# Optimization experiments

Hardware: AMD Instinct MI355X
Metric: run time of the kernel (lower is better)

Reference implementation:

```python
import jax, jax.numpy as jnp
import numpy as np

BETA = 1.0  # config.beta
B, G, K, E2 = 1024, 512, 128, 128


def setup_inputs() -> dict:
    key = jax.random.key(0)
    k1, k2, k3, k4, k5 = jax.random.split(key, 5)
    s = 0.05
    return {
        "images": jax.random.normal(k1, (B, G), dtype=jnp.float32),
        "wimg": jax.random.normal(k2, (G, K), dtype=jnp.float32) * s,    # project.weight.T
        "wrec": jax.random.normal(k3, (K, E2), dtype=jnp.float32) * s,   # rec.weight.T
        "wrec2": jax.random.normal(k4, (K + 1, E2), dtype=jnp.float32) * s,  # rec2.weight.T
        "wimg2": jax.random.normal(k5, (G, K, K + 1), dtype=jnp.float32) * s,  # img2.weight.T.reshape(K+1,K,G).T
    }


def _soft_assign(x, codes):
    # x: [B, D], codes: [D, C] -> softmax over C of -beta * mean_D (x - codes)^2
    xh = -jnp.mean((x[:, :, None] - codes[None]) ** 2, axis=1) * BETA  # [B, C]
    return jax.nn.softmax(xh, axis=-1)


def reference(images, wimg, wrec, wrec2, wimg2):
    # ---- encode ----
    xp = _soft_assign(images, wimg)            # [B, K]
    lat = xp @ wrec                            # [B, E2]
    xp = _soft_assign(lat, wrec.T)             # [B, K] (codes are wrec.T: [E2, K])
    idx = jnp.argmax(xp, axis=-1)              # [B] hard component
    xwimg = jnp.transpose(wimg2[:, idx, :], (1, 0, 2))   # [B, G, K+1]
    base = wimg[:, idx].T[:, :, None]                     # [B, G, 1]
    xd = images[:, :, None] - base - xwimg                # [B, G, K+1]
    xh2 = -jnp.mean(xd ** 2, axis=1) * BETA               # [B, K+1]
    xp2 = jax.nn.softmax(xh2, axis=-1)
    lat2 = xp2 @ wrec2                                    # [B, E2]
    # ---- decode (ret='rec', n_step>=1) ----
    xp_d = _soft_assign(lat, wrec.T)           # [B, K]
    xp2_d = _soft_assign(lat2, wrec2.T)        # [B, K+1]
    wimgg = wimg[:, :, None] + wimg2           # [G, K, K+1]
    # tensordot(xp_d[:, :, None]*xp2_d[:, None, :], wimgg.permute(1,2,0), 2)
    xrec = jnp.einsum('bk,bj,gkj->bg', xp_d, xp2_d, wimgg)  # [B, G]
    # ---- loss ----
    loss = jnp.mean((xrec - images) ** 2, axis=-1)  # [B]
    return loss
```

## Files before the change

kernel.cpp:

```cpp
#include <hip/hip_runtime.h>

#define B_    1024
#define G_    512
#define K_    128
#define J_    129
#define JP_   132
#define E2_   128
#define KK_   16512
#define KK2_  16896
#define KKE2_ 17024
#define KKP_  17408
#define SPLITS 16
#define KCHUNK 1088
#define BK_   32
#define KSTEPS 34
#define GS_   8

using short8 = __attribute__((ext_vector_type(8))) short;
using f32x4  = __attribute__((ext_vector_type(4))) float;

__device__ __forceinline__ float bf2f(unsigned short h){
  return __uint_as_float(((unsigned int)h) << 16);
}
__device__ __forceinline__ unsigned short f2bf(float f){
  unsigned int u = __float_as_uint(f);
  u += 0x7fffu + ((u >> 16) & 1u);
  return (unsigned short)(u >> 16);
}

#define GLOAD16(gptr, ldst) __builtin_amdgcn_global_load_lds( \
    (const __attribute__((address_space(1))) unsigned int*)(gptr), \
    (__attribute__((address_space(3))) unsigned int*)(ldst), 16, 0, 0)

__device__ __forceinline__ void blockSum2(float v0, float v1, float* red, int t,
                                          float& r0, float& r1){
  #pragma unroll
  for (int off = 32; off > 0; off >>= 1){
    v0 += __shfl_down(v0, off);
    v1 += __shfl_down(v1, off);
  }
  __syncthreads();
  if ((t & 63) == 0){ red[t >> 6] = v0; red[8 + (t >> 6)] = v1; }
  __syncthreads();
  r0 = ((red[0] + red[1]) + (red[2] + red[3])) + ((red[4] + red[5]) + (red[6] + red[7]));
  r1 = ((red[8] + red[9]) + (red[10] + red[11])) + ((red[12] + red[13]) + (red[14] + red[15]));
  __syncthreads();
}

__device__ __forceinline__ void blockSoftmaxMS2(float x0, float x1, bool act,
    float* redm, float* reds, int t,
    float& m0o, float& s0o, float& m1o, float& s1o){
  float m0 = x0, s0 = act ? 1.f : 0.f;
  float m1 = x1, s1 = act ? 1.f : 0.f;
  #pragma unroll
  for (int off = 32; off > 0; off >>= 1){
    float om0 = __shfl_down(m0, off), os0 = __shfl_down(s0, off);
    float om1 = __shfl_down(m1, off), os1 = __shfl_down(s1, off);
    float nm0 = fmaxf(m0, om0);
    s0 = s0*__expf(m0 - nm0) + os0*__expf(om0 - nm0); m0 = nm0;
    float nm1 = fmaxf(m1, om1);
    s1 = s1*__expf(m1 - nm1) + os1*__expf(om1 - nm1); m1 = nm1;
  }
  __syncthreads();
  if ((t & 63) == 0){
    redm[t >> 6] = m0; reds[t >> 6] = s0;
    redm[8 + (t >> 6)] = m1; reds[8 + (t >> 6)] = s1;
  }
  __syncthreads();
  float gm0 = redm[0], gs0 = reds[0], gm1 = redm[8], gs1 = reds[8];
  #pragma unroll
  for (int w = 1; w < 8; w++){
    float om0 = redm[w], os0 = reds[w];
    float nm0 = fmaxf(gm0, om0);
    gs0 = gs0*__expf(gm0 - nm0) + os0*__expf(om0 - nm0); gm0 = nm0;
    float om1 = redm[8 + w], os1 = reds[8 + w];
    float nm1 = fmaxf(gm1, om1);
    gs1 = gs1*__expf(gm1 - nm1) + os1*__expf(om1 - nm1); gm1 = nm1;
  }
  m0o = gm0; s0o = gs0; m1o = gm1; s1o = gs1;
}

__device__ __forceinline__ void blockSoftmaxMSI2(float x0, float x1, int idx, bool act,
    float* redm, float* reds, int* redi, int t,
    float& m0o, float& s0o, int& i0o, float& m1o, float& s1o, int& i1o){
  float m0 = x0, s0 = act ? 1.f : 0.f; int i0 = idx;
  float m1 = x1, s1 = act ? 1.f : 0.f; int i1 = idx;
  #pragma unroll
  for (int off = 32; off > 0; off >>= 1){
    float om0 = __shfl_down(m0, off), os0 = __shfl_down(s0, off);
    int   oi0 = __shfl_down(i0, off);
    float om1 = __shfl_down(m1, off), os1 = __shfl_down(s1, off);
    int   oi1 = __shfl_down(i1, off);
    bool tk0 = (om0 > m0) || (om0 == m0 && oi0 < i0);
    float nm0 = fmaxf(m0, om0);
    s0 = s0*__expf(m0 - nm0) + os0*__expf(om0 - nm0);
    i0 = tk0 ? oi0 : i0; m0 = nm0;
    bool tk1 = (om1 > m1) || (om1 == m1 && oi1 < i1);
    float nm1 = fmaxf(m1, om1);
    s1 = s1*__expf(m1 - nm1) + os1*__expf(om1 - nm1);
    i1 = tk1 ? oi1 : i1; m1 = nm1;
  }
  __syncthreads();
  if ((t & 63) == 0){
    redm[t >> 6] = m0; reds[t >> 6] = s0; redi[t >> 6] = i0;
    redm[8 + (t >> 6)] = m1; reds[8 + (t >> 6)] = s1; redi[8 + (t >> 6)] = i1;
  }
  __syncthreads();
  float gm0 = redm[0], gs0 = reds[0]; int gi0 = redi[0];
  float gm1 = redm[8], gs1 = reds[8]; int gi1 = redi[8];
  #pragma unroll
  for (int w = 1; w < 8; w++){
    { float om = redm[w], os = reds[w]; int oi = redi[w];
      bool tk = (om > gm0) || (om == gm0 && oi < gi0);
      float nm = fmaxf(gm0, om);
      gs0 = gs0*__expf(gm0 - nm) + os*__expf(om - nm);
      gi0 = tk ? oi : gi0; gm0 = nm; }
    { float om = redm[8 + w], os = reds[8 + w]; int oi = redi[8 + w];
      bool tk = (om > gm1) || (om == gm1 && oi < gi1);
      float nm = fmaxf(gm1, om);
      gs1 = gs1*__expf(gm1 - nm) + os*__expf(om - nm);
      gi1 = tk ? oi : gi1; gm1 = nm; }
  }
  m0o = gm0; s0o = gs0; i0o = gi0; m1o = gm1; s1o = gs1; i1o = gi1;
}

__global__ __launch_bounds__(1024) void norms_kernel(
    const float* __restrict__ wimg, const float* __restrict__ wrec,
    const float* __restrict__ wrec2, float* __restrict__ c1norm,
    float* __restrict__ w3norm, float* __restrict__ w6norm,
    float* __restrict__ wrecT, float* __restrict__ wrec2T){
  int t = threadIdx.x;
  if (blockIdx.x == 0){
    __shared__ float red[8][128];
    int k = t & 127, sl = t >> 7;
    float s = 0.f;
    int g0 = sl * (G_/8);
    for (int g = g0; g < g0 + G_/8; g++){
      float v = wimg[g*K_ + k]; s += v*v;
    }
    red[sl][k] = s;
    __syncthreads();
    if (t < 128){
      float r = 0.f;
      #pragma unroll
      for (int i = 0; i < 8; i++) r += red[i][t];
      c1norm[t] = r;
    }
  } else if (blockIdx.x == 1){
    int wave = t >> 6, lane = t & 63;
    for (int k = wave; k < K_; k += 16){
      float v0 = wrec[k*E2_ + lane], v1 = wrec[k*E2_ + 64 + lane];
      float s = v0*v0 + v1*v1;
      #pragma unroll
      for (int off = 32; off > 0; off >>= 1) s += __shfl_down(s, off);
      if (lane == 0) w3norm[k] = s;
    }
  } else if (blockIdx.x == 2){
    int wave = t >> 6, lane = t & 63;
    for (int j = wave; j < J_; j += 16){
      float v0 = wrec2[j*E2_ + lane], v1 = wrec2[j*E2_ + 64 + lane];
      float s = v0*v0 + v1*v1;
      #pragma unroll
      for (int off = 32; off > 0; off >>= 1) s += __shfl_down(s, off);
      if (lane == 0) w6norm[j] = s;
    }
  } else if (blockIdx.x == 3){
    for (int n = t; n < K_*E2_; n += 1024){
      int k = n >> 7, e = n & 127;
      wrecT[e*K_ + k] = wrec[n];
    }
  } else {
    for (int n = t; n < J_*E2_; n += 1024){
      int j = n >> 7, e = n & 127;
      wrec2T[e*J_ + j] = wrec2[n];
    }
  }
}

__global__ __launch_bounds__(128) void tables_part_kernel(
    const float* __restrict__ wimg2, const float* __restrict__ wimg,
    float* __restrict__ sqp, float* __restrict__ crp,
    unsigned short* __restrict__ W2){
  int n  = blockIdx.x * 128 + threadIdx.x;
  int gs = blockIdx.y;
  int k = n / J_;
  int w2i = n + 3*k;
  float s0=0,s1=0,s2=0,s3=0, c0=0,c1=0,c2=0,c3=0;
  int gbase = gs * (G_/GS_);
  #pragma unroll 2
  for (int g = gbase; g < gbase + G_/GS_; g += 4){
    float w0 = wimg2[(size_t)(g  )*KK_ + n];
    float w1 = wimg2[(size_t)(g+1)*KK_ + n];
    float w2 = wimg2[(size_t)(g+2)*KK_ + n];
    float w3 = wimg2[(size_t)(g+3)*KK_ + n];
    W2[(size_t)(g  )*KKP_ + w2i] = f2bf(w0);
    W2[(size_t)(g+1)*KKP_ + w2i] = f2bf(w1);
    W2[(size_t)(g+2)*KKP_ + w2i] = f2bf(w2);
    W2[(size_t)(g+3)*KKP_ + w2i] = f2bf(w3);
    s0 += w0*w0; s1 += w1*w1; s2 += w2*w2; s3 += w3*w3;
    c0 += wimg[(g  )*K_ + k]*w0;
    c1 += wimg[(g+1)*K_ + k]*w1;
    c2 += wimg[(g+2)*K_ + k]*w2;
    c3 += wimg[(g+3)*K_ + k]*w3;
  }
  sqp[(size_t)gs*KK_ + n] = (s0+s1)+(s2+s3);
  crp[(size_t)gs*KK_ + n] = (c0+c1)+(c2+c3);
}
__global__ __launch_bounds__(128) void tables_reduce_kernel(
    const float* __restrict__ sqp, const float* __restrict__ crp,
    float* __restrict__ sq2, float* __restrict__ cross){
  int n = blockIdx.x * 128 + threadIdx.x;
  float s = 0.f, c = 0.f;
  #pragma unroll
  for (int gs = 0; gs < GS_; gs++){
    s += sqp[(size_t)gs*KK_ + n];
    c += crp[(size_t)gs*KK_ + n];
  }
  sq2[n] = s; cross[n] = c;
}

__global__ __launch_bounds__(128) void w2tail_kernel(
    const float* __restrict__ wimg, unsigned short* __restrict__ W2){
  int g = blockIdx.x, t = threadIdx.x;
  unsigned short* dst = W2 + (size_t)g * KKP_;
  dst[KK2_ + t]        = f2bf(wimg[g*K_ + t]);
  dst[KKE2_ + t]       = 0;
  dst[KKE2_ + 128 + t] = 0;
  dst[KKE2_ + 256 + t] = 0;
  dst[t*JP_ + 129] = 0;
  dst[t*JP_ + 130] = 0;
  dst[t*JP_ + 131] = 0;
}

__global__ __launch_bounds__(512, 4) void encdec_kernel(
    const float* __restrict__ img,  const float* __restrict__ wimg,
    const float* __restrict__ wrec, const float* __restrict__ wrec2,
    const float* __restrict__ wrecT, const float* __restrict__ wrec2T,
    const unsigned short* __restrict__ W2,
    const float* __restrict__ c1norm, const float* __restrict__ w3norm,
    const float* __restrict__ w6norm, const float* __restrict__ sq2,
    const float* __restrict__ cross, unsigned short* __restrict__ Rm){
  __shared__ __align__(16) float simg[2][G_];
  __shared__ float sp[2][K_];
  __shared__ float sqv[2][JP_];
  __shared__ float slat[2][E2_];
  __shared__ float sd1[2][K_];
  __shared__ __align__(16) float sh16a[16][128];
  __shared__ __align__(16) float sh16b[16][128];
  __shared__ float sh4a[4][K_], sh4b[4][K_];
  __shared__ float xtra[4];
  __shared__ float redm[16], reds[16];
  __shared__ int   redi[16];

  int t = threadIdx.x;
  int b0 = blockIdx.x * 2, b1 = b0 + 1;
  int tt = t & 127, q = t >> 7;
  int ll = t & 31, gq = t >> 5;
  int wvid = t >> 6, lane = t & 63;

  simg[0][t] = img[b0*G_ + t];
  simg[1][t] = img[b1*G_ + t];
  __syncthreads();
  float a0 = simg[0][t], a1 = simg[1][t];
  float in0, in1;
  blockSum2(a0*a0, a1*a1, redm, t, in0, in1);

  {
    float p00=0,p01=0,p02=0,p03=0, p10=0,p11=0,p12=0,p13=0;
    int g0 = gq * 32;
    #pragma unroll 4
    for (int g = g0; g < g0 + 32; g++){
      float4 wv = *(const float4*)(wimg + g*K_ + 4*ll);
      float sv0 = simg[0][g], sv1 = simg[1][g];
      p00 += sv0*wv.x; p01 += sv0*wv.y; p02 += sv0*wv.z; p03 += sv0*wv.w;
      p10 += sv1*wv.x; p11 += sv1*wv.y; p12 += sv1*wv.z; p13 += sv1*wv.w;
    }
    float4 st0 = {p00,p01,p02,p03};
    float4 st1 = {p10,p11,p12,p13};
    *(float4*)&sh16a[gq][4*ll] = st0;
    *(float4*)&sh16b[gq][4*ll] = st1;
  }
  __syncthreads();
  float xh10 = -3e38f, xh11 = -3e38f;
  if (t < 128){
    float d0 = 0.f, d1 = 0.f;
    #pragma unroll
    for (int i = 0; i < 16; i++){ d0 += sh16a[i][t]; d1 += sh16b[i][t]; }
    sd1[0][t] = d0; sd1[1][t] = d1;
    xh10 = -(in0 - 2.f*d0 + c1norm[t]) * (1.f/512.f);
    xh11 = -(in1 - 2.f*d1 + c1norm[t]) * (1.f/512.f);
  }
  float m10, s10, m11, s11;
  blockSoftmaxMS2(xh10, xh11, t < 128, redm, reds, t, m10, s10, m11, s11);
  if (t < 128){
    sp[0][t] = __expf(xh10 - m10) / s10;
    sp[1][t] = __expf(xh11 - m11) / s11;
  }
  __syncthreads();

  {
    float l00=0,l01=0, l10=0,l11=0;
    int k0 = q * 32;
    for (int k = k0; k < k0 + 32; k += 2){
      float w0 = wrec[(k  )*E2_ + tt];
      float w1 = wrec[(k+1)*E2_ + tt];
      l00 += sp[0][k]*w0; l01 += sp[0][k+1]*w1;
      l10 += sp[1][k]*w0; l11 += sp[1][k+1]*w1;
    }
    sh4a[q][tt] = l00 + l01;
    sh4b[q][tt] = l10 + l11;
  }
  __syncthreads();
  float lat0 = (sh4a[0][tt] + sh4a[1][tt]) + (sh4a[2][tt] + sh4a[3][tt]);
  float lat1 = (sh4b[0][tt] + sh4b[1][tt]) + (sh4b[2][tt] + sh4b[3][tt]);
  if (q == 0){ slat[0][tt] = lat0; slat[1][tt] = lat1; }
  float ln0, ln1;
  blockSum2((q == 0) ? lat0*lat0 : 0.f, (q == 0) ? lat1*lat1 : 0.f, redm, t, ln0, ln1);

  {
    float l00=0,l01=0, l10=0,l11=0;
    int e0 = q * 32;
    const float* rT = wrecT + tt;
    for (int e = e0; e < e0 + 32; e += 2){
      float w0 = rT[(e  )*K_];
      float w1 = rT[(e+1)*K_];
      l00 += slat[0][e]*w0; l01 += slat[0][e+1]*w1;
      l10 += slat[1][e]*w0; l11 += slat[1][e+1]*w1;
    }
    sh4a[q][tt] = l00 + l01;
    sh4b[q][tt] = l10 + l11;
  }
  __syncthreads();
  float xh30 = -3e38f, xh31 = -3e38f;
  if (t < 128){
    float d30 = (sh4a[0][t] + sh4a[1][t]) + (sh4a[2][t] + sh4a[3][t]);
    float d31 = (sh4b[0][t] + sh4b[1][t]) + (sh4b[2][t] + sh4b[3][t]);
    xh30 = -(ln0 - 2.f*d30 + w3norm[t]) * (1.f/128.f);
    xh31 = -(ln1 - 2.f*d31 + w3norm[t]) * (1.f/128.f);
  }
  float m30, s30, m31, s31; int idx0, idx1;
  blockSoftmaxMSI2(xh30, xh31, tt, t < 128, redm, reds, redi, t,
                   m30, s30, idx0, m31, s31, idx1);
  if (t < 128){
    sp[0][t] = __expf(xh30 - m30) / s30;
    sp[1][t] = __expf(xh31 - m31) / s31;
  }
  float dsq0 = in0 - 2.f*sd1[0][idx0] + c1norm[idx0];
  float dsq1 = in1 - 2.f*sd1[1][idx1] + c1norm[idx1];

  {
    const unsigned short* Wb0 = W2 + (size_t)idx0 * JP_ + 4*ll;
    const unsigned short* Wb1 = W2 + (size_t)idx1 * JP_ + 4*ll;
    float p00=0,p01=0,p02=0,p03=0, p10=0,p11=0,p12=0,p13=0;
    int g0 = gq * 32;
    #pragma unroll 2
    for (int g = g0; g < g0 + 32; g++){
      uint2 w0 = *(const uint2*)(Wb0 + (size_t)g*KKP_);
      uint2 w1 = *(const uint2*)(Wb1 + (size_t)g*KKP_);
      float sv0 = simg[0][g], sv1 = simg[1][g];
      p00 += sv0 * __uint_as_float(w0.x << 16);
      p01 += sv0 * __uint_as_float(w0.x & 0xffff0000u);
      p02 += sv0 * __uint_as_float(w0.y << 16);
      p03 += sv0 * __uint_as_float(w0.y & 0xffff0000u);
      p10 += sv1 * __uint_as_float(w1.x << 16);
      p11 += sv1 * __uint_as_float(w1.x & 0xffff0000u);
      p12 += sv1 * __uint_as_float(w1.y << 16);
      p13 += sv1 * __uint_as_float(w1.y & 0xffff0000u);
    }
    float4 st0 = {p00,p01,p02,p03};
    float4 st1 = {p10,p11,p12,p13};
    *(float4*)&sh16a[gq][4*ll] = st0;
    *(float4*)&sh16b[gq][4*ll] = st1;
  }
  if (wvid < 2){
    int ib = wvid ? idx1 : idx0;
    const float* si = simg[wvid];
    const unsigned short* Wb8 = W2 + (size_t)ib * JP_ + 128;
    float s = 0.f;
    #pragma unroll
    for (int m = 0; m < 8; m++){
      int g = lane + 64*m;
      s += si[g] * bf2f(Wb8[(size_t)g * KKP_]);
    }
    #pragma unroll
    for (int off = 32; off > 0; off >>= 1) s += __shfl_down(s, off);
    if (lane == 0) xtra[wvid] = s;
  }
  __syncthreads();
  float xh20 = -3e38f, xh21 = -3e38f;
  if (t < J_){
    float di0, di1;
    if (t < 128){
      di0 = 0.f; di1 = 0.f;
      #pragma unroll
      for (int i = 0; i < 16; i++){ di0 += sh16a[i][t]; di1 += sh16b[i][t]; }
    } else { di0 = xtra[0]; di1 = xtra[1]; }
    int nb0 = idx0*J_ + t, nb1 = idx1*J_ + t;
    xh20 = -(dsq0 - 2.f*(di0 - cross[nb0]) + sq2[nb0]) * (1.f/512.f);
    xh21 = -(dsq1 - 2.f*(di1 - cross[nb1]) + sq2[nb1]) * (1.f/512.f);
  }
  float m20, s20, m21, s21;
  blockSoftmaxMS2(xh20, xh21, t < J_, redm, reds, t, m20, s20, m21, s21);
  if (t < J_){
    sqv[0][t] = __expf(xh20 - m20) / s20;
    sqv[1][t] = __expf(xh21 - m21) / s21;
  }
  __syncthreads();

  {
    float lv0 = 0.f, lv1 = 0.f;
    int j0 = (q == 0) ? 0 : (q*32 + 1);
    int j1 = q*32 + 33;
    for (int j = j0; j < j1; j++){
      float w = wrec2[j*E2_ + tt];
      lv0 += sqv[0][j]*w; lv1 += sqv[1][j]*w;
    }
    sh4a[q][tt] = lv0;
    sh4b[q][tt] = lv1;
  }
  __syncthreads();
  float l20 = (sh4a[0][tt] + sh4a[1][tt]) + (sh4a[2][tt] + sh4a[3][tt]);
  float l21 = (sh4b[0][tt] + sh4b[1][tt]) + (sh4b[2][tt] + sh4b[3][tt]);
  if (q == 0){ slat[0][tt] = l20; slat[1][tt] = l21; }
  float n20, n21;
  blockSum2((q == 0) ? l20*l20 : 0.f, (q == 0) ? l21*l21 : 0.f, redm, t, n20, n21);

  {
    float l00=0,l01=0, l10=0,l11=0;
    int e0 = q * 32;
    const float* rT = wrec2T + tt;
    for (int e = e0; e < e0 + 32; e += 2){
      float w0 = rT[(e  )*J_];
      float w1 = rT[(e+1)*J_];
      l00 += slat[0][e]*w0; l01 += slat[0][e+1]*w1;
      l10 += slat[1][e]*w0; l11 += slat[1][e+1]*w1;
    }
    sh4a[q][tt] = l00 + l01;
    sh4b[q][tt] = l10 + l11;
  }
  if (wvid < 2){
    const float* sl = slat[wvid];
    float s = sl[lane]*wrec2T[lane*J_ + 128] + sl[lane+64]*wrec2T[(lane+64)*J_ + 128];
    #pragma unroll
    for (int off = 32; off > 0; off >>= 1) s += __shfl_down(s, off);
    if (lane == 0) xtra[2 + wvid] = s;
  }
  __syncthreads();
  float xh60 = -3e38f, xh61 = -3e38f;
  if (t < J_){
    float d60, d61;
    if (t < 128){
      d60 = (sh4a[0][t] + sh4a[1][t]) + (sh4a[2][t] + sh4a[3][t]);
      d61 = (sh4b[0][t] + sh4b[1][t]) + (sh4b[2][t] + sh4b[3][t]);
    } else { d60 = xtra[2]; d61 = xtra[3]; }
    xh60 = -(n20 - 2.f*d60 + w6norm[t]) * (1.f/128.f);
    xh61 = -(n21 - 2.f*d61 + w6norm[t]) * (1.f/128.f);
  }
  float m60, s60, m61, s61;
  blockSoftmaxMS2(xh60, xh61, t < J_, redm, reds, t, m60, s60, m61, s61);
  if (t < J_){
    sqv[0][t] = __expf(xh60 - m60) / s60;
    sqv[1][t] = __expf(xh61 - m61) / s61;
  }
  __syncthreads();

  unsigned int* R0 = (unsigned int*)(Rm + (size_t)b0 * KKP_);
  unsigned int* R1 = (unsigned int*)(Rm + (size_t)b1 * KKP_);
  int k = t / 66;
  int j2 = t - k*66;
  for (int kk2 = t; kk2 < KKP_/2; kk2 += 512){
    float v00 = 0.f, v01 = 0.f, v10 = 0.f, v11 = 0.f;
    if (kk2 < KK2_/2){
      int j = 2*j2;
      float pk0 = sp[0][k], pk1 = sp[1][k];
      bool jo0 = (j < J_), jo1 = (j+1 < J_);
      v00 = jo0 ? pk0 * sqv[0][j]   : 0.f;
      v01 = jo1 ? pk0 * sqv[0][j+1] : 0.f;
      v10 = jo0 ? pk1 * sqv[1][j]   : 0.f;
      v11 = jo1 ? pk1 * sqv[1][j+1] : 0.f;
    } else if (kk2 < KKE2_/2){
      int e = 2*(kk2 - KK2_/2);
      v00 = sp[0][e]; v01 = sp[0][e+1];
      v10 = sp[1][e]; v11 = sp[1][e+1];
    }
    R0[kk2] = (unsigned int)f2bf(v00) | ((unsigned int)f2bf(v01) << 16);
    R1[kk2] = (unsigned int)f2bf(v10) | ((unsigned int)f2bf(v11) << 16);
    j2 += 50;
    if (j2 >= 66){ j2 -= 66; k += 8; } else k += 7;
  }
}

__global__ __launch_bounds__(256) void gemm_kernel(
    const unsigned short* __restrict__ Rm, const unsigned short* __restrict__ W2,
    float* __restrict__ part){
  __shared__ __align__(16) unsigned int lds[8192];
  auto lds3 = (__attribute__((address_space(3))) unsigned int*)lds;
  int tid = threadIdx.x;
  int l = tid & 63;
  int wv = tid >> 6;
  int wr = (wv >> 1) * 64, wc = (wv & 1) * 64;
  int b0 = blockIdx.y * 128, g0 = blockIdx.x * 128;
  size_t kkbase = (size_t)blockIdx.z * KCHUNK;

  int srow = tid >> 2, scol = tid & 3;
  const unsigned short* ga  = Rm + (size_t)(b0 + srow)*KKP_ + kkbase + scol*8;
  const unsigned short* ga2 = ga + (size_t)64 * KKP_;
  const unsigned short* gb  = W2 + (size_t)(g0 + srow)*KKP_ + kkbase + scol*8;
  const unsigned short* gb2 = gb + (size_t)64 * KKP_;

  int lrow = l & 15, lko = (l >> 4) << 2;

  f32x4 zero4 = {0.f, 0.f, 0.f, 0.f};
  f32x4 acc[4][4];
  #pragma unroll
  for (int mi = 0; mi < 4; mi++)
    #pragma unroll
    for (int ni = 0; ni < 4; ni++) acc[mi][ni] = zero4;

  GLOAD16(ga,  lds3 + wv*256);
  GLOAD16(ga2, lds3 + 1024 + wv*256);
  GLOAD16(gb,  lds3 + 2048 + wv*256);
  GLOAD16(gb2, lds3 + 3072 + wv*256);
  ga += BK_; ga2 += BK_; gb += BK_; gb2 += BK_;

  int cur = 0;
  for (int s = 0; s < KSTEPS; s++){
    __syncthreads();
    if (s + 1 < KSTEPS){
      unsigned int nb = (cur ^ 1) * 4096;
      GLOAD16(ga,  lds3 + nb + wv*256);
      GLOAD16(ga2, lds3 + nb + 1024 + wv*256);
      GLOAD16(gb,  lds3 + nb + 2048 + wv*256);
      GLOAD16(gb2, lds3 + nb + 3072 + wv*256);
      ga += BK_; ga2 += BK_; gb += BK_; gb2 += BK_;
    }
    const unsigned int* lA = lds + cur*4096;
    const unsigned int* lB = lA + 2048;
    short8 af[4], bfv[4];
    #pragma unroll
    for (int mi = 0; mi < 4; mi++)
      af[mi] = *(const short8*)(lA + (wr + mi*16 + lrow)*16 + lko);
    #pragma unroll
    for (int ni = 0; ni < 4; ni++)
      bfv[ni] = *(const short8*)(lB + (wc + ni*16 + lrow)*16 + lko);
    #pragma unroll
    for (int mi = 0; mi < 4; mi++)
      #pragma unroll
      for (int ni = 0; ni < 4; ni++)
        acc[mi][ni] = __builtin_amdgcn_mfma_f32_16x16x32_bf16(af[mi], bfv[ni], acc[mi][ni], 0, 0, 0);
    cur ^= 1;
  }

  float* P = part + ((size_t)blockIdx.z * B_ + b0) * G_ + g0;
  int rh = (l >> 4) << 2, cl = l & 15;
  #pragma unroll
  for (int mi = 0; mi < 4; mi++)
    #pragma unroll
    for (int ni = 0; ni < 4; ni++)
      #pragma unroll
      for (int r = 0; r < 4; r++){
        int row = wr + mi*16 + rh + r;
        int col = wc + ni*16 + cl;
        P[(size_t)row*G_ + col] = acc[mi][ni][r];
      }
}

__global__ __launch_bounds__(128) void loss_kernel(
    const float* __restrict__ img, const float* __restrict__ part,
    float* __restrict__ out){
  __shared__ float redf[2];
  int t = threadIdx.x, b = blockIdx.x;
  float acc = 0.f;
  for (int g = t; g < G_; g += 128){
    float x = 0.f;
    #pragma unroll
    for (int z = 0; z < SPLITS; z++)
      x += part[((size_t)z*B_ + b)*G_ + g];
    float d = x - img[b*G_ + g];
    acc += d*d;
  }
  #pragma unroll
  for (int off = 32; off > 0; off >>= 1) acc += __shfl_down(acc, off);
  __syncthreads();
  if ((t & 63) == 0) redf[t >> 6] = acc;
  __syncthreads();
  if (t == 0) out[b] = (redf[0] + redf[1]) * (1.f/512.f);
}

extern "C" void kernel_launch(void* const* d_in, const int* in_sizes, int n_in,
                              void* d_out, int out_size, void* d_ws, size_t ws_size,
                              hipStream_t stream){
  (void)in_sizes; (void)n_in; (void)out_size; (void)ws_size;
  const float* img   = (const float*)d_in[0];
  const float* wimg  = (const float*)d_in[1];
  const float* wrec  = (const float*)d_in[2];
  const float* wrec2 = (const float*)d_in[3];
  const float* wimg2 = (const float*)d_in[4];
  float* out = (float*)d_out;

  char* ws = (char*)d_ws;
  size_t off = 0;
  auto alloc = [&](size_t bytes) -> void* {
    void* p = ws + off;
    off += (bytes + 255) & ~(size_t)255;
    return p;
  };
  unsigned short* W2   = (unsigned short*)alloc((size_t)G_ * KKP_ * 2);
  unsigned short* Rm   = (unsigned short*)alloc((size_t)B_ * KKP_ * 2);
  float* part   = (float*)alloc((size_t)SPLITS * B_ * G_ * 4);
  float* sqp    = (float*)alloc((size_t)GS_ * KK_ * 4);
  float* crp    = (float*)alloc((size_t)GS_ * KK_ * 4);
  float* sq2    = (float*)alloc((size_t)KK_ * 4);
  float* cross  = (float*)alloc((size_t)KK_ * 4);
  float* c1norm = (float*)alloc(K_ * 4);
  float* w3norm = (float*)alloc(K_ * 4);
  float* w6norm = (float*)alloc(J_ * 4);
  float* wrecT  = (float*)alloc((size_t)K_ * E2_ * 4);
  float* wrec2T = (float*)alloc((size_t)J_ * E2_ * 4);

  norms_kernel<<<dim3(5), dim3(1024), 0, stream>>>(wimg, wrec, wrec2, c1norm, w3norm, w6norm, wrecT, wrec2T);
  tables_part_kernel<<<dim3(129, GS_), dim3(128), 0, stream>>>(wimg2, wimg, sqp, crp, W2);
  tables_reduce_kernel<<<dim3(129), dim3(128), 0, stream>>>(sqp, crp, sq2, cross);
  w2tail_kernel<<<dim3(512), dim3(128), 0, stream>>>(wimg, W2);
  encdec_kernel<<<dim3(512), dim3(512), 0, stream>>>(img, wimg, wrec, wrec2, wrecT, wrec2T, W2,
      c1norm, w3norm, w6norm, sq2, cross, Rm);
  gemm_kernel<<<dim3(4, 8, SPLITS), dim3(256), 0, stream>>>(Rm, W2, part);
  loss_kernel<<<dim3(1024), dim3(128), 0, stream>>>(img, part, out);
}
```

Measured before the change: 116.4 us.

## Double GEMM K-tile with XOR-swizzled LDS and store split-K partials as bf16

The GEMM K-step doubles from 32 to 64, halving the number of barrier/prefetch iterations, and the LDS layout becomes XOR-swizzled to avoid bank conflicts on the wider rows. Split-K partial sums are written as bf16 instead of fp32, halving partial-buffer traffic, and the loss kernel reads them with vectorized loads. This adds rounding error to each of the 16 partials before summation and doubles LDS use per block, which may reduce occupancy.

```diff
diff --git a/kernel.cpp b/kernel.cpp
--- a/kernel.cpp
+++ b/kernel.cpp
@@ -12,8 +12,8 @@
 #define KKP_  17408
 #define SPLITS 16
 #define KCHUNK 1088
-#define BK_   32
-#define KSTEPS 34
+#define BK_   64
+#define KSTEPS 17
 #define GS_   8
 
 using short8 = __attribute__((ext_vector_type(8))) short;
@@ -492,8 +492,8 @@
 
 __global__ __launch_bounds__(256) void gemm_kernel(
     const unsigned short* __restrict__ Rm, const unsigned short* __restrict__ W2,
-    float* __restrict__ part){
-  __shared__ __align__(16) unsigned int lds[8192];
+    unsigned short* __restrict__ part){
+  __shared__ __align__(16) unsigned int lds[16384];
   auto lds3 = (__attribute__((address_space(3))) unsigned int*)lds;
   int tid = threadIdx.x;
   int l = tid & 63;
@@ -502,13 +502,12 @@
   int b0 = blockIdx.y * 128, g0 = blockIdx.x * 128;
   size_t kkbase = (size_t)blockIdx.z * KCHUNK;
 
-  int srow = tid >> 2, scol = tid & 3;
-  const unsigned short* ga  = Rm + (size_t)(b0 + srow)*KKP_ + kkbase + scol*8;
-  const unsigned short* ga2 = ga + (size_t)64 * KKP_;
-  const unsigned short* gb  = W2 + (size_t)(g0 + srow)*KKP_ + kkbase + scol*8;
-  const unsigned short* gb2 = gb + (size_t)64 * KKP_;
-
-  int lrow = l & 15, lko = (l >> 4) << 2;
+  int srow = tid >> 3;
+  int cswz = (tid & 7) ^ (srow & 7);
+  const unsigned short* ga = Rm + (size_t)(b0 + srow)*KKP_ + kkbase + cswz*8;
+  const unsigned short* gb = W2 + (size_t)(g0 + srow)*KKP_ + kkbase + cswz*8;
+
+  int lrow = l & 15, lh = l >> 4, p7 = l & 7;
 
   f32x4 zero4 = {0.f, 0.f, 0.f, 0.f};
   f32x4 acc[4][4];
@@ -517,41 +516,43 @@
     #pragma unroll
     for (int ni = 0; ni < 4; ni++) acc[mi][ni] = zero4;
 
-  GLOAD16(ga,  lds3 + wv*256);
-  GLOAD16(ga2, lds3 + 1024 + wv*256);
-  GLOAD16(gb,  lds3 + 2048 + wv*256);
-  GLOAD16(gb2, lds3 + 3072 + wv*256);
-  ga += BK_; ga2 += BK_; gb += BK_; gb2 += BK_;
-
+  auto STAGE = [&](int bb){
+    unsigned int base = bb * 8192;
+    #pragma unroll
+    for (int c = 0; c < 4; c++){
+      GLOAD16(ga + (size_t)c*32*KKP_, lds3 + base + c*1024 + wv*256);
+      GLOAD16(gb + (size_t)c*32*KKP_, lds3 + base + 4096 + c*1024 + wv*256);
+    }
+    ga += BK_; gb += BK_;
+  };
+
+  STAGE(0);
   int cur = 0;
   for (int s = 0; s < KSTEPS; s++){
     __syncthreads();
-    if (s + 1 < KSTEPS){
-      unsigned int nb = (cur ^ 1) * 4096;
-      GLOAD16(ga,  lds3 + nb + wv*256);
-      GLOAD16(ga2, lds3 + nb + 1024 + wv*256);
-      GLOAD16(gb,  lds3 + nb + 2048 + wv*256);
-      GLOAD16(gb2, lds3 + nb + 3072 + wv*256);
-      ga += BK_; ga2 += BK_; gb += BK_; gb2 += BK_;
-    }
-    const unsigned int* lA = lds + cur*4096;
-    const unsigned int* lB = lA + 2048;
-    short8 af[4], bfv[4];
-    #pragma unroll
-    for (int mi = 0; mi < 4; mi++)
-      af[mi] = *(const short8*)(lA + (wr + mi*16 + lrow)*16 + lko);
-    #pragma unroll
-    for (int ni = 0; ni < 4; ni++)
-      bfv[ni] = *(const short8*)(lB + (wc + ni*16 + lrow)*16 + lko);
-    #pragma unroll
-    for (int mi = 0; mi < 4; mi++)
+    if (s + 1 < KSTEPS) STAGE(cur ^ 1);
+    const unsigned int* lA = lds + cur*8192;
+    const unsigned int* lB = lA + 4096;
+    #pragma unroll
+    for (int s2 = 0; s2 < 2; s2++){
+      int slot = ((s2 << 2) + lh) ^ p7;
+      short8 af[4], bfv[4];
+      #pragma unroll
+      for (int mi = 0; mi < 4; mi++)
+        af[mi] = *(const short8*)(lA + (wr + mi*16 + lrow)*32 + slot*4);
       #pragma unroll
       for (int ni = 0; ni < 4; ni++)
-        acc[mi][ni] = __builtin_amdgcn_mfma_f32_16x16x32_bf16(af[mi], bfv[ni], acc[mi][ni], 0, 0, 0);
+        bfv[ni] = *(const short8*)(lB + (wc + ni*16 + lrow)*32 + slot*4);
+      #pragma unroll
+      for (int mi = 0; mi < 4; mi++)
+        #pragma unroll
+        for (int ni = 0; ni < 4; ni++)
+          acc[mi][ni] = __builtin_amdgcn_mfma_f32_16x16x32_bf16(af[mi], bfv[ni], acc[mi][ni], 0, 0, 0);
+    }
     cur ^= 1;
   }
 
-  float* P = part + ((size_t)blockIdx.z * B_ + b0) * G_ + g0;
+  unsigned short* P = part + ((size_t)blockIdx.z * B_ + b0) * G_ + g0;
   int rh = (l >> 4) << 2, cl = l & 15;
   #pragma unroll
   for (int mi = 0; mi < 4; mi++)
@@ -561,24 +562,28 @@
       for (int r = 0; r < 4; r++){
         int row = wr + mi*16 + rh + r;
         int col = wc + ni*16 + cl;
-        P[(size_t)row*G_ + col] = acc[mi][ni][r];
+        P[(size_t)row*G_ + col] = f2bf(acc[mi][ni][r]);
       }
 }
 
 __global__ __launch_bounds__(128) void loss_kernel(
-    const float* __restrict__ img, const float* __restrict__ part,
+    const float* __restrict__ img, const unsigned short* __restrict__ part,
     float* __restrict__ out){
   __shared__ float redf[2];
   int t = threadIdx.x, b = blockIdx.x;
-  float acc = 0.f;
-  for (int g = t; g < G_; g += 128){
-    float x = 0.f;
-    #pragma unroll
-    for (int z = 0; z < SPLITS; z++)
-      x += part[((size_t)z*B_ + b)*G_ + g];
-    float d = x - img[b*G_ + g];
-    acc += d*d;
-  }
+  float x0 = 0.f, x1 = 0.f, x2 = 0.f, x3 = 0.f;
+  #pragma unroll
+  for (int z = 0; z < SPLITS; z++){
+    const unsigned short* pr = part + ((size_t)z*B_ + b)*G_ + 4*t;
+    uint2 v = *(const uint2*)pr;
+    x0 += __uint_as_float(v.x << 16);
+    x1 += __uint_as_float(v.x & 0xffff0000u);
+    x2 += __uint_as_float(v.y << 16);
+    x3 += __uint_as_float(v.y & 0xffff0000u);
+  }
+  float4 iv = *(const float4*)(img + (size_t)b*G_ + 4*t);
+  float d0 = x0 - iv.x, d1 = x1 - iv.y, d2 = x2 - iv.z, d3 = x3 - iv.w;
+  float acc = (d0*d0 + d1*d1) + (d2*d2 + d3*d3);
   #pragma unroll
   for (int off = 32; off > 0; off >>= 1) acc += __shfl_down(acc, off);
   __syncthreads();
@@ -607,7 +612,7 @@
   };
   unsigned short* W2   = (unsigned short*)alloc((size_t)G_ * KKP_ * 2);
   unsigned short* Rm   = (unsigned short*)alloc((size_t)B_ * KKP_ * 2);
-  float* part   = (float*)alloc((size_t)SPLITS * B_ * G_ * 4);
+  unsigned short* part = (unsigned short*)alloc((size_t)SPLITS * B_ * G_ * 2);
   float* sqp    = (float*)alloc((size_t)GS_ * KK_ * 4);
   float* crp    = (float*)alloc((size_t)GS_ * KK_ * 4);
   float* sq2    = (float*)alloc((size_t)KK_ * 4);
```

After: 113.9 us. 2.2% less time.
